# Kernel optimization log

Hardware: AMD Instinct MI355X
Metric: run time of the kernel (lower is better)

## Reference

```python
import jax, jax.numpy as jnp
import numpy as np

B, T, K = 512, 1024, 48          # batch, seq_len, n_tokens
START, END = 46, 47              # token_dict['START'], token_dict['END']
NEG = -10000.0


def setup_inputs() -> dict:
    key = jax.random.key(0)
    k1, k2 = jax.random.split(key)
    feats = jax.random.normal(k1, (B, T, K), dtype=jnp.float32)
    transitions = jax.random.normal(k2, (K, K), dtype=jnp.float32)
    return {"feats": feats, "transitions": transitions}


def _mask_transitions(transitions):
    # Mirrors __init__: no transition out of END-column target / into START row.
    t = transitions.at[START, :].set(NEG)
    t = t.at[:, END].set(NEG)
    return t


def _crf_logz(feats, trans):
    """forward_prop: CRF forward algorithm. feats [T,K], trans [K_next,K_prev]."""
    init = jnp.full((K,), NEG, feats.dtype).at[START].set(0.0)

    def step(alpha, feat):
        # scores[next, prev] = alpha[prev] + trans[next, prev] + feat[next]
        scores = alpha[None, :] + trans + feat[:, None]
        return jax.nn.logsumexp(scores, axis=1), None

    alpha, _ = jax.lax.scan(step, init, feats)
    return jax.nn.logsumexp(alpha + trans[END])


def _viterbi(feats, trans):
    """viterbi_decode: max-product recurrence + backtrace. feats [T,K]."""
    init = jnp.full((K,), NEG, feats.dtype).at[START].set(0.0)

    def step(v, feat):
        # NOTE: original takes argmax BEFORE adding emission, then adds feat.
        scores = v[None, :] + trans          # [K_next, K_prev]
        bp = jnp.argmax(scores, axis=1)      # backpointers [K]
        return jnp.max(scores, axis=1) + feat, bp

    v, bptrs = jax.lax.scan(step, init, feats)   # bptrs [T, K]
    term = v + trans[END]
    last = jnp.argmax(term)
    path_score = term[last]

    def back(tag, bp):
        return bp[tag], tag

    _, path = jax.lax.scan(back, last, bptrs, reverse=True)  # path [T]
    return path_score, path


def reference(feats, transitions):
    trans = _mask_transitions(transitions)
    logz = jax.vmap(lambda f: _crf_logz(f, trans))(feats)          # [B]
    scores, paths = jax.vmap(lambda f: _viterbi(f, trans))(feats)  # [B], [B,T]
    return logz, scores, paths
```

## Files before the change

### kernel.cpp

```cpp
#include <hip/hip_runtime.h>

#define NB 512
#define NT 1024
#define NK 48
#define NEGV -10000.0f
#define S_START 46
#define S_END 47

__device__ __forceinline__ float rfl_f32(float x) {
    return __int_as_float(__builtin_amdgcn_readfirstlane(__float_as_int(x)));
}

extern "C" __global__ __launch_bounds__(128, 1)
void crf_fused(const float* __restrict__ feats, const float* __restrict__ trans,
               float* __restrict__ out)
{
    __shared__ unsigned char bp[NT * NK];
    __shared__ unsigned char comp[64 * NK];
    __shared__ unsigned char boundary[64];
    __shared__ float eabuf[64];
    __shared__ float vbuf[64];

    const int b = blockIdx.x;
    const int wave = threadIdx.x >> 6;
    const int lane = threadIdx.x & 63;
    const bool act = lane < NK;
    const int LL = act ? lane : (NK - 1);
    const float* f = feats + (size_t)b * NT * NK;
    const float* fb = f + LL;

    float tEnd = NEGV;
    if (act && lane != S_END) tEnd = trans[S_END * NK + lane];

    if (wave == 0) {
        float Erow[NK];
        {
            const bool rowdead = (lane == S_START);
            const float4* r4 = (const float4*)(trans + LL * NK);
            #pragma unroll
            for (int q = 0; q < NK / 4; ++q) {
                float4 r = r4[q];
                const int c = 4 * q;
                Erow[c + 0] = (rowdead || c + 0 == S_END) ? 0.0f : __expf(r.x);
                Erow[c + 1] = (rowdead || c + 1 == S_END) ? 0.0f : __expf(r.y);
                Erow[c + 2] = (rowdead || c + 2 == S_END) ? 0.0f : __expf(r.z);
                Erow[c + 3] = (rowdead || c + 3 == S_END) ? 0.0f : __expf(r.w);
            }
        }
        float u = (lane == S_START) ? 0.0f : NEGV;
        float Muni = 0.0f;
        eabuf[lane] = __expf(u);
        __builtin_amdgcn_wave_barrier();

        float fr0 = fb[0 * NK], fr1 = fb[1 * NK], fr2 = fb[2 * NK], fr3 = fb[3 * NK];

        auto fstep = [&](float fc) {
            float ea[NK];
            {
                const float4* e4 = (const float4*)eabuf;
                #pragma unroll
                for (int q = 0; q < NK / 4; ++q) {
                    float4 r = e4[q];
                    ea[4 * q + 0] = r.x; ea[4 * q + 1] = r.y;
                    ea[4 * q + 2] = r.z; ea[4 * q + 3] = r.w;
                }
            }
            float a0 = 0.f, a1 = 0.f, a2 = 0.f, a3 = 0.f;
            #pragma unroll
            for (int p = 0; p < NK; p += 4) {
                a0 = fmaf(Erow[p + 0], ea[p + 0], a0);
                a1 = fmaf(Erow[p + 1], ea[p + 1], a1);
                a2 = fmaf(Erow[p + 2], ea[p + 2], a2);
                a3 = fmaf(Erow[p + 3], ea[p + 3], a3);
            }
            float acc = (a0 + a1) + (a2 + a3);
            float w = __logf(acc) + fc;
            float dM = rfl_f32(w);
            Muni += dM;
            u = w - dM;
            __builtin_amdgcn_wave_barrier();
            eabuf[lane] = __expf(u);
            __builtin_amdgcn_wave_barrier();
        };

        for (int t = 0; t < NT; t += 4) {
            { float fc = fr0; int nr = (t + 4 < NT) ? t + 4 : NT - 1; fr0 = fb[nr * NK]; fstep(fc); }
            { float fc = fr1; int nr = (t + 5 < NT) ? t + 5 : NT - 1; fr1 = fb[nr * NK]; fstep(fc); }
            { float fc = fr2; int nr = (t + 6 < NT) ? t + 6 : NT - 1; fr2 = fb[nr * NK]; fstep(fc); }
            { float fc = fr3; int nr = (t + 7 < NT) ? t + 7 : NT - 1; fr3 = fb[nr * NK]; fstep(fc); }
        }
        float x = act ? (u + tEnd) : -INFINITY;
        float M2 = x;
        #pragma unroll
        for (int off = 32; off >= 1; off >>= 1)
            M2 = fmaxf(M2, __shfl_xor(M2, off, 64));
        float e = __expf(x - M2);
        #pragma unroll
        for (int off = 32; off >= 1; off >>= 1)
            e += __shfl_xor(e, off, 64);
        if (lane == 0) out[b] = Muni + M2 + __logf(e);
    } else {
        float trow[NK];
        {
            const bool rowdead = (lane == S_START);
            const float4* r4 = (const float4*)(trans + LL * NK);
            #pragma unroll
            for (int q = 0; q < NK / 4; ++q) {
                float4 r = r4[q];
                const int c = 4 * q;
                trow[c + 0] = (rowdead || c + 0 == S_END) ? NEGV : r.x;
                trow[c + 1] = (rowdead || c + 1 == S_END) ? NEGV : r.y;
                trow[c + 2] = (rowdead || c + 2 == S_END) ? NEGV : r.z;
                trow[c + 3] = (rowdead || c + 3 == S_END) ? NEGV : r.w;
            }
        }
        float v = (lane == S_START) ? 0.0f : NEGV;
        vbuf[lane] = v;
        __builtin_amdgcn_wave_barrier();

        float fr0 = fb[0 * NK], fr1 = fb[1 * NK], fr2 = fb[2 * NK], fr3 = fb[3 * NK];
        const int big = 63;

        auto vstep = [&](float fc, int tt) {
            float s[NK];
            {
                const float4* v4 = (const float4*)vbuf;
                #pragma unroll
                for (int q = 0; q < NK / 4; ++q) {
                    float4 r = v4[q];
                    s[4 * q + 0] = r.x + trow[4 * q + 0];
                    s[4 * q + 1] = r.y + trow[4 * q + 1];
                    s[4 * q + 2] = r.z + trow[4 * q + 2];
                    s[4 * q + 3] = r.w + trow[4 * q + 3];
                }
            }
            float m16[16];
            #pragma unroll
            for (int i = 0; i < 16; ++i)
                m16[i] = fmaxf(fmaxf(s[3 * i], s[3 * i + 1]), s[3 * i + 2]);
            float m6[6];
            #pragma unroll
            for (int i = 0; i < 5; ++i)
                m6[i] = fmaxf(fmaxf(m16[3 * i], m16[3 * i + 1]), m16[3 * i + 2]);
            m6[5] = m16[15];
            float best = fmaxf(fmaxf(fmaxf(m6[0], m6[1]), m6[2]),
                               fmaxf(fmaxf(m6[3], m6[4]), m6[5]));
            int ix[NK];
            #pragma unroll
            for (int p = 0; p < NK; ++p)
                ix[p] = (s[p] != best) ? big : p;
            int n16[16];
            #pragma unroll
            for (int i = 0; i < 16; ++i)
                n16[i] = min(min(ix[3 * i], ix[3 * i + 1]), ix[3 * i + 2]);
            int n6[6];
            #pragma unroll
            for (int i = 0; i < 5; ++i)
                n6[i] = min(min(n16[3 * i], n16[3 * i + 1]), n16[3 * i + 2]);
            n6[5] = n16[15];
            int bi = min(min(min(n6[0], n6[1]), n6[2]),
                         min(min(n6[3], n6[4]), n6[5]));

            bp[tt * NK + LL] = (unsigned char)bi;
            v = best + fc;
            __builtin_amdgcn_wave_barrier();
            vbuf[lane] = v;
            __builtin_amdgcn_wave_barrier();
        };

        for (int t = 0; t < NT; t += 4) {
            { float fc = fr0; int nr = (t + 4 < NT) ? t + 4 : NT - 1; fr0 = fb[nr * NK]; vstep(fc, t + 0); }
            { float fc = fr1; int nr = (t + 5 < NT) ? t + 5 : NT - 1; fr1 = fb[nr * NK]; vstep(fc, t + 1); }
            { float fc = fr2; int nr = (t + 6 < NT) ? t + 6 : NT - 1; fr2 = fb[nr * NK]; vstep(fc, t + 2); }
            { float fc = fr3; int nr = (t + 7 < NT) ? t + 7 : NT - 1; fr3 = fb[nr * NK]; vstep(fc, t + 3); }
        }
        float xv = act ? (v + tEnd) : -INFINITY;
        int idx = act ? lane : 63;
        float val = xv;
        #pragma unroll
        for (int off = 32; off >= 1; off >>= 1) {
            float ov = __shfl_xor(val, off, 64);
            int   oi = __shfl_xor(idx, off, 64);
            if (ov > val || (ov == val && oi < idx)) { val = ov; idx = oi; }
        }
        if (lane == 0) out[NB + b] = val;
        const int last = idx;

        __builtin_amdgcn_wave_barrier();
        int cur[NK];
        #pragma unroll
        for (int k = 0; k < NK; ++k) cur[k] = k;
        const int tbase = lane * 16;
        for (int i = 15; i >= 0; --i) {
            const int t = tbase + i;
            #pragma unroll
            for (int k = 0; k < NK; ++k) cur[k] = bp[t * NK + cur[k]];
        }
        #pragma unroll
        for (int k = 0; k < NK; ++k) comp[lane * NK + k] = (unsigned char)cur[k];
        __builtin_amdgcn_wave_barrier();

        if (lane == 0) {
            int tag = last;
            for (int l = 63; l >= 0; --l) {
                boundary[l] = (unsigned char)tag;
                tag = comp[l * NK + tag];
            }
        }
        __builtin_amdgcn_wave_barrier();

        int tag = boundary[lane];
        float* pout = out + 2 * NB + (size_t)b * NT;
        for (int i = 15; i >= 0; --i) {
            const int t = tbase + i;
            pout[t] = (float)tag;
            tag = bp[t * NK + tag];
        }
    }
}

extern "C" void kernel_launch(void* const* d_in, const int* in_sizes, int n_in,
                              void* d_out, int out_size, void* d_ws, size_t ws_size,
                              hipStream_t stream) {
    (void)in_sizes; (void)n_in; (void)d_ws; (void)ws_size; (void)out_size;
    const float* feats = (const float*)d_in[0];
    const float* trans = (const float*)d_in[1];
    float* out = (float*)d_out;
    crf_fused<<<dim3(NB), dim3(128), 0, stream>>>(feats, trans, out);
}
```

Measured before the change: 521.4 us.

## Shorten recurrence critical paths by dropping wave barriers and reordering LDS stores

The forward (logsumexp) wave no longer renormalizes with a readfirstlane of its own result. Each lane now takes the max of the previous exp-values it already loads from LDS and uses its log as the shift, so the normalization is computed alongside the FMAs. The Viterbi wave writes its new score to LDS right after computing the max, before the argmax index search, so the next step's data is ready sooner. All wave_barrier scheduling fences are removed, which frees the compiler to reorder work. The cost is reliance on in-order LDS within a single wave and on compiler alias ordering, plus slightly different numerics from the new normalization.

```diff
diff --git a/kernel.cpp b/kernel.cpp
--- a/kernel.cpp
+++ b/kernel.cpp
@@ -6,10 +6,6 @@
 #define NEGV -10000.0f
 #define S_START 46
 #define S_END 47
-
-__device__ __forceinline__ float rfl_f32(float x) {
-    return __int_as_float(__builtin_amdgcn_readfirstlane(__float_as_int(x)));
-}
 
 extern "C" __global__ __launch_bounds__(128, 1)
 void crf_fused(const float* __restrict__ feats, const float* __restrict__ trans,
@@ -50,37 +46,32 @@
         float u = (lane == S_START) ? 0.0f : NEGV;
         float Muni = 0.0f;
         eabuf[lane] = __expf(u);
-        __builtin_amdgcn_wave_barrier();
 
         float fr0 = fb[0 * NK], fr1 = fb[1 * NK], fr2 = fb[2 * NK], fr3 = fb[3 * NK];
 
         auto fstep = [&](float fc) {
-            float ea[NK];
-            {
-                const float4* e4 = (const float4*)eabuf;
-                #pragma unroll
-                for (int q = 0; q < NK / 4; ++q) {
-                    float4 r = e4[q];
-                    ea[4 * q + 0] = r.x; ea[4 * q + 1] = r.y;
-                    ea[4 * q + 2] = r.z; ea[4 * q + 3] = r.w;
-                }
-            }
+            const float4* e4 = (const float4*)eabuf;
             float a0 = 0.f, a1 = 0.f, a2 = 0.f, a3 = 0.f;
-            #pragma unroll
-            for (int p = 0; p < NK; p += 4) {
-                a0 = fmaf(Erow[p + 0], ea[p + 0], a0);
-                a1 = fmaf(Erow[p + 1], ea[p + 1], a1);
-                a2 = fmaf(Erow[p + 2], ea[p + 2], a2);
-                a3 = fmaf(Erow[p + 3], ea[p + 3], a3);
+            float mq[12];
+            #pragma unroll
+            for (int q = 0; q < 12; ++q) {
+                float4 r = e4[q];
+                a0 = fmaf(Erow[4 * q + 0], r.x, a0);
+                a1 = fmaf(Erow[4 * q + 1], r.y, a1);
+                a2 = fmaf(Erow[4 * q + 2], r.z, a2);
+                a3 = fmaf(Erow[4 * q + 3], r.w, a3);
+                mq[q] = fmaxf(fmaxf(r.x, r.y), fmaxf(r.z, r.w));
             }
             float acc = (a0 + a1) + (a2 + a3);
-            float w = __logf(acc) + fc;
-            float dM = rfl_f32(w);
+            float m01 = fmaxf(fmaxf(mq[0], mq[1]), fmaxf(mq[2], mq[3]));
+            float m23 = fmaxf(fmaxf(mq[4], mq[5]), fmaxf(mq[6], mq[7]));
+            float m45 = fmaxf(fmaxf(mq[8], mq[9]), fmaxf(mq[10], mq[11]));
+            float m_e = fmaxf(fmaxf(m01, m23), m45);
+
+            float dM = __logf(m_e);
+            u = __logf(acc) + fc - dM;
+            eabuf[lane] = __expf(u);
             Muni += dM;
-            u = w - dM;
-            __builtin_amdgcn_wave_barrier();
-            eabuf[lane] = __expf(u);
-            __builtin_amdgcn_wave_barrier();
         };
 
         for (int t = 0; t < NT; t += 4) {
@@ -116,7 +107,6 @@
         }
         float v = (lane == S_START) ? 0.0f : NEGV;
         vbuf[lane] = v;
-        __builtin_amdgcn_wave_barrier();
 
         float fr0 = fb[0 * NK], fr1 = fb[1 * NK], fr2 = fb[2 * NK], fr3 = fb[3 * NK];
         const int big = 63;
@@ -145,6 +135,10 @@
             m6[5] = m16[15];
             float best = fmaxf(fmaxf(fmaxf(m6[0], m6[1]), m6[2]),
                                fmaxf(fmaxf(m6[3], m6[4]), m6[5]));
+
+            v = best + fc;
+            vbuf[lane] = v;
+
             int ix[NK];
             #pragma unroll
             for (int p = 0; p < NK; ++p)
@@ -160,12 +154,7 @@
             n6[5] = n16[15];
             int bi = min(min(min(n6[0], n6[1]), n6[2]),
                          min(min(n6[3], n6[4]), n6[5]));
-
             bp[tt * NK + LL] = (unsigned char)bi;
-            v = best + fc;
-            __builtin_amdgcn_wave_barrier();
-            vbuf[lane] = v;
-            __builtin_amdgcn_wave_barrier();
         };
 
         for (int t = 0; t < NT; t += 4) {
```

Result: slower. 634.8 us (+21.7%).
